# Kernel tuning notes

Hardware: AMD Instinct MI355X
Metric: run time of the kernel (lower is better)

Reference implementation:

```python
import jax, jax.numpy as jnp
import numpy as np

I_DIM = 50000
D_DIM = 128
N_EDGES = 800000
N_NODES = I_DIM + 1


def setup_inputs() -> dict:
    key = jax.random.key(0)
    k1, k2, k3, k4 = jax.random.split(key, 4)
    # edge[:,0] must be sorted for the original bincount+repeat normalization to be valid
    src = jnp.sort(jax.random.randint(k1, (N_EDGES,), 0, N_NODES))
    dst = jax.random.randint(k2, (N_EDGES,), 0, N_NODES)
    edge = jnp.stack([src, dst], axis=1).astype(jnp.int64)
    # GlorotNormal-style init for the embedding table and dense layers
    emb_mat = jax.random.normal(k3, (N_NODES, D_DIM), dtype=jnp.float32) * np.sqrt(2.0 / (N_NODES + D_DIM))
    kA, kB = jax.random.split(k4)
    W_scale = jax.random.normal(kA, (D_DIM, D_DIM), dtype=jnp.float32) * np.sqrt(2.0 / (2 * D_DIM))
    b_scale = jnp.zeros((D_DIM,), dtype=jnp.float32)
    W_att = jax.random.normal(kB, (2 * D_DIM, 1), dtype=jnp.float32) * np.sqrt(2.0 / (2 * D_DIM + 1))
    b_att = jnp.zeros((1,), dtype=jnp.float32)
    return {"edge": edge, "emb_mat": emb_mat, "W_scale": W_scale,
            "b_scale": b_scale, "W_att": W_att, "b_att": b_att}


def reference(edge, emb_mat, W_scale, b_scale, W_att, b_att):
    E = edge.shape[0]
    src = edge[:, 0]
    dst = edge[:, 1]
    # gather both endpoints, project: [E, 2, d]
    edge_emb = jnp.einsum('epd,df->epf', emb_mat[edge], W_scale) + b_scale
    edge_emb = edge_emb.reshape(E, -1)                       # [E, 2d]
    att = edge_emb @ W_att + b_att                           # [E, 1]
    att = jnp.where(att >= 0, att, 0.2 * att)                # LeakyReLU(0.2)
    att = jnp.squeeze(att, axis=-1)                          # [E]
    scores = jnp.exp(att - 1.0)
    score_sum = jax.ops.segment_sum(scores, src, num_segments=N_NODES)
    score_norm = scores / score_sum[src]                     # segment softmax
    item_scaled = emb_mat @ W_scale + b_scale                # [N, d]
    msgs = score_norm[:, None] * item_scaled[dst]            # [E, d]
    agg = jax.ops.segment_sum(msgs, src, num_segments=N_NODES)
    return jax.nn.sigmoid(agg)                               # [N, d]
```

## Files before the change

### kernel.cpp

```cpp
#include <hip/hip_runtime.h>
#include <math.h>

#define NN 50001
#define DD 128
#define NE 800000

typedef __attribute__((ext_vector_type(8))) short short8;
typedef __attribute__((ext_vector_type(4))) float floatx4;

__device__ __forceinline__ unsigned short f2bf(float f) {
    unsigned u = __builtin_bit_cast(unsigned, f);
    u += 0x7fffu + ((u >> 16) & 1u);
    return (unsigned short)(u >> 16);
}
__device__ __forceinline__ float bflo(unsigned u) {
    return __builtin_bit_cast(float, u << 16);
}
__device__ __forceinline__ float bfhi(unsigned u) {
    return __builtin_bit_cast(float, u & 0xffff0000u);
}
__device__ __forceinline__ float score(float att) {
    att = att >= 0.f ? att : 0.2f * att;
    return __expf(att - 1.f);
}

__global__ void k_prep(const float* __restrict__ W, unsigned short* __restrict__ WT,
                       const int* __restrict__ edge, int* __restrict__ row_ptr) {
    int b = blockIdx.x;
    if (b < 64) {
        int idx = b * 256 + threadIdx.x;
        int k = idx >> 7, j = idx & 127;
        WT[j * DD + k] = f2bf(W[idx]);
    } else {
        int e = (b - 64) * 256 + threadIdx.x;
        if (e >= NE) return;
        int s = edge[2 * e];
        if (e == 0) {
            for (int n = 0; n <= s; n++) row_ptr[n] = 0;
        } else {
            int p = edge[2 * (e - 1)];
            for (int n = p + 1; n <= s; n++) row_ptr[n] = e;
        }
        if (e == NE - 1) {
            for (int n = s + 1; n <= NN; n++) row_ptr[n] = NE;
        }
    }
}

__global__ void __launch_bounds__(256) k_gemm(const float* __restrict__ emb,
        const unsigned short* __restrict__ WT, const float* __restrict__ b_scale,
        const float* __restrict__ W_att, unsigned short* __restrict__ item,
        float* __restrict__ a_src, float* __restrict__ a_dst) {
    int wave = blockIdx.x * 4 + (threadIdx.x >> 6);
    int lane = threadIdx.x & 63;
    int base = wave * 16;
    if (base >= NN) return;
    int m = lane & 15, q = lane >> 4;

    int row = base + m; if (row >= NN) row = NN - 1;
    const float* ap = emb + (long)row * DD + q * 8;
    short8 a[4];
    #pragma unroll
    for (int ks = 0; ks < 4; ks++) {
        float4 f0 = *(const float4*)(ap + ks * 32);
        float4 f1 = *(const float4*)(ap + ks * 32 + 4);
        a[ks][0] = (short)f2bf(f0.x); a[ks][1] = (short)f2bf(f0.y);
        a[ks][2] = (short)f2bf(f0.z); a[ks][3] = (short)f2bf(f0.w);
        a[ks][4] = (short)f2bf(f1.x); a[ks][5] = (short)f2bf(f1.y);
        a[ks][6] = (short)f2bf(f1.z); a[ks][7] = (short)f2bf(f1.w);
    }

    float p_src[4] = {0.f, 0.f, 0.f, 0.f};
    float p_dst[4] = {0.f, 0.f, 0.f, 0.f};

    #pragma unroll
    for (int ft = 0; ft < 8; ft++) {
        int col = ft * 16 + m;
        floatx4 acc = {0.f, 0.f, 0.f, 0.f};
        #pragma unroll
        for (int ks = 0; ks < 4; ks++) {
            short8 b = *(const short8*)(WT + col * DD + ks * 32 + q * 8);
            acc = __builtin_amdgcn_mfma_f32_16x16x32_bf16(a[ks], b, acc, 0, 0, 0);
        }
        float bs = b_scale[col];
        float wsrc = W_att[col], wdst = W_att[DD + col];
        #pragma unroll
        for (int r = 0; r < 4; r++) {
            float v = acc[r] + bs;
            int gr = base + q * 4 + r;
            if (gr < NN) item[(long)gr * DD + col] = f2bf(v);
            p_src[r] += v * wsrc;
            p_dst[r] += v * wdst;
        }
    }
    #pragma unroll
    for (int off = 1; off <= 8; off <<= 1) {
        #pragma unroll
        for (int r = 0; r < 4; r++) {
            p_src[r] += __shfl_xor(p_src[r], off, 64);
            p_dst[r] += __shfl_xor(p_dst[r], off, 64);
        }
    }
    if (m == 0) {
        #pragma unroll
        for (int r = 0; r < 4; r++) {
            int gr = base + q * 4 + r;
            if (gr < NN) { a_src[gr] = p_src[r]; a_dst[gr] = p_dst[r]; }
        }
    }
}

__global__ void __launch_bounds__(256) k_agg(const int* __restrict__ edge,
        const int* __restrict__ row_ptr, const unsigned short* __restrict__ item,
        const float* __restrict__ a_src, const float* __restrict__ a_dst,
        const float* __restrict__ b_att, float* __restrict__ out) {
    int n = blockIdx.x * 4 + (threadIdx.x >> 6);
    int lane = threadIdx.x & 63;
    if (n >= NN) return;
    int g = lane >> 4, t = lane & 15;

    int start = row_ptr[n];
    int len = row_ptr[n + 1] - start;
    const int* dp = edge + 2 * start + 1;

    if (len > 0) {
        float asrc = a_src[n] + b_att[0];
        float acc[8] = {0.f, 0.f, 0.f, 0.f, 0.f, 0.f, 0.f, 0.f};
        float ssum = 0.f;
        int j = g;
        for (; j + 12 < len; j += 16) {
            int d0 = dp[2 * j], d1 = dp[2 * (j + 4)], d2 = dp[2 * (j + 8)], d3 = dp[2 * (j + 12)];
            float x0 = a_dst[d0], x1 = a_dst[d1], x2 = a_dst[d2], x3 = a_dst[d3];
            uint4 u0 = *(const uint4*)(item + (long)d0 * DD + t * 8);
            uint4 u1 = *(const uint4*)(item + (long)d1 * DD + t * 8);
            uint4 u2 = *(const uint4*)(item + (long)d2 * DD + t * 8);
            uint4 u3 = *(const uint4*)(item + (long)d3 * DD + t * 8);
            float s0 = score(asrc + x0), s1 = score(asrc + x1);
            float s2 = score(asrc + x2), s3 = score(asrc + x3);
            ssum += (s0 + s1) + (s2 + s3);
            acc[0] += s0 * bflo(u0.x); acc[1] += s0 * bfhi(u0.x);
            acc[2] += s0 * bflo(u0.y); acc[3] += s0 * bfhi(u0.y);
            acc[4] += s0 * bflo(u0.z); acc[5] += s0 * bfhi(u0.z);
            acc[6] += s0 * bflo(u0.w); acc[7] += s0 * bfhi(u0.w);
            acc[0] += s1 * bflo(u1.x); acc[1] += s1 * bfhi(u1.x);
            acc[2] += s1 * bflo(u1.y); acc[3] += s1 * bfhi(u1.y);
            acc[4] += s1 * bflo(u1.z); acc[5] += s1 * bfhi(u1.z);
            acc[6] += s1 * bflo(u1.w); acc[7] += s1 * bfhi(u1.w);
            acc[0] += s2 * bflo(u2.x); acc[1] += s2 * bfhi(u2.x);
            acc[2] += s2 * bflo(u2.y); acc[3] += s2 * bfhi(u2.y);
            acc[4] += s2 * bflo(u2.z); acc[5] += s2 * bfhi(u2.z);
            acc[6] += s2 * bflo(u2.w); acc[7] += s2 * bfhi(u2.w);
            acc[0] += s3 * bflo(u3.x); acc[1] += s3 * bfhi(u3.x);
            acc[2] += s3 * bflo(u3.y); acc[3] += s3 * bfhi(u3.y);
            acc[4] += s3 * bflo(u3.z); acc[5] += s3 * bfhi(u3.z);
            acc[6] += s3 * bflo(u3.w); acc[7] += s3 * bfhi(u3.w);
        }
        for (; j < len; j += 4) {
            int d = dp[2 * j];
            float x = a_dst[d];
            uint4 u = *(const uint4*)(item + (long)d * DD + t * 8);
            float s = score(asrc + x);
            ssum += s;
            acc[0] += s * bflo(u.x); acc[1] += s * bfhi(u.x);
            acc[2] += s * bflo(u.y); acc[3] += s * bfhi(u.y);
            acc[4] += s * bflo(u.z); acc[5] += s * bfhi(u.z);
            acc[6] += s * bflo(u.w); acc[7] += s * bfhi(u.w);
        }
        #pragma unroll
        for (int off = 16; off <= 32; off <<= 1) {
            #pragma unroll
            for (int k = 0; k < 8; k++) acc[k] += __shfl_xor(acc[k], off, 64);
            ssum += __shfl_xor(ssum, off, 64);
        }
        float inv = 1.f / ssum;
        float4 o;
        if (g == 0) {
            o.x = 1.f / (1.f + __expf(-acc[0] * inv));
            o.y = 1.f / (1.f + __expf(-acc[1] * inv));
            o.z = 1.f / (1.f + __expf(-acc[2] * inv));
            o.w = 1.f / (1.f + __expf(-acc[3] * inv));
            *(float4*)(out + (long)n * DD + t * 8) = o;
        } else if (g == 1) {
            o.x = 1.f / (1.f + __expf(-acc[4] * inv));
            o.y = 1.f / (1.f + __expf(-acc[5] * inv));
            o.z = 1.f / (1.f + __expf(-acc[6] * inv));
            o.w = 1.f / (1.f + __expf(-acc[7] * inv));
            *(float4*)(out + (long)n * DD + t * 8 + 4) = o;
        }
    } else {
        float4 h = make_float4(0.5f, 0.5f, 0.5f, 0.5f);
        if (g == 0)      *(float4*)(out + (long)n * DD + t * 8) = h;
        else if (g == 1) *(float4*)(out + (long)n * DD + t * 8 + 4) = h;
    }
}

extern "C" void kernel_launch(void* const* d_in, const int* in_sizes, int n_in,
                              void* d_out, int out_size, void* d_ws, size_t ws_size,
                              hipStream_t stream) {
    const int*   edge    = (const int*)d_in[0];
    const float* emb     = (const float*)d_in[1];
    const float* W_scale = (const float*)d_in[2];
    const float* b_scale = (const float*)d_in[3];
    const float* W_att   = (const float*)d_in[4];
    const float* b_att   = (const float*)d_in[5];
    float* out = (float*)d_out;

    char* ws = (char*)d_ws;
    unsigned short* WT      = (unsigned short*)(ws);
    int*            row_ptr = (int*)(ws + 32768);
    float*          a_src   = (float*)(ws + 233600);
    float*          a_dst   = (float*)(ws + 433792);
    unsigned short* item    = (unsigned short*)(ws + 633984);

    int node_blocks = (NN + 3) / 4;
    int tile_blocks = ((NN + 15) / 16 + 3) / 4;
    int edge_blocks = (NE + 255) / 256;

    k_prep <<<64 + edge_blocks, 256, 0, stream>>>(W_scale, WT, edge, row_ptr);
    k_gemm <<<tile_blocks,      256, 0, stream>>>(emb, WT, b_scale, W_att, item, a_src, a_dst);
    k_agg  <<<node_blocks,      256, 0, stream>>>(edge, row_ptr, item, a_src, a_dst, b_att, out);
}
```

Baseline: 146.8 us.

## Move row_ptr build into GEMM launch and transpose MFMA operands for vector stores

Row-pointer construction now runs in extra blocks of the GEMM kernel instead of the prep kernel, so the prep kernel only transposes W and the heavy edge scan overlaps with the GEMM. The MFMA operands are swapped so each lane holds four consecutive output features of one node. That allows packed 8-byte bf16 stores of item, float4 loads of bias and attention weights, and a shorter cross-lane reduction. The GEMM launch grows, and GEMM and edge blocks now compete for the same CUs.

```diff
diff --git a/kernel.cpp b/kernel.cpp
--- a/kernel.cpp
+++ b/kernel.cpp
@@ -4,6 +4,8 @@
 #define NN 50001
 #define DD 128
 #define NE 800000
+#define GEMM_BLOCKS 782
+#define EDGE_BLOCKS 3125
 
 typedef __attribute__((ext_vector_type(8))) short short8;
 typedef __attribute__((ext_vector_type(4))) float floatx4;
@@ -24,15 +26,19 @@
     return __expf(att - 1.f);
 }
 
-__global__ void k_prep(const float* __restrict__ W, unsigned short* __restrict__ WT,
-                       const int* __restrict__ edge, int* __restrict__ row_ptr) {
-    int b = blockIdx.x;
-    if (b < 64) {
-        int idx = b * 256 + threadIdx.x;
-        int k = idx >> 7, j = idx & 127;
-        WT[j * DD + k] = f2bf(W[idx]);
-    } else {
-        int e = (b - 64) * 256 + threadIdx.x;
+__global__ void k_prep(const float* __restrict__ W, unsigned short* __restrict__ WT) {
+    int idx = blockIdx.x * 256 + threadIdx.x;
+    int k = idx >> 7, j = idx & 127;
+    WT[j * DD + k] = f2bf(W[idx]);
+}
+
+__global__ void __launch_bounds__(256) k_gemm(const float* __restrict__ emb,
+        const unsigned short* __restrict__ WT, const float* __restrict__ b_scale,
+        const float* __restrict__ W_att, const int* __restrict__ edge,
+        unsigned short* __restrict__ item, float* __restrict__ a_src,
+        float* __restrict__ a_dst, int* __restrict__ row_ptr) {
+    if (blockIdx.x >= GEMM_BLOCKS) {
+        int e = (blockIdx.x - GEMM_BLOCKS) * 256 + threadIdx.x;
         if (e >= NE) return;
         int s = edge[2 * e];
         if (e == 0) {
@@ -44,70 +50,58 @@
         if (e == NE - 1) {
             for (int n = s + 1; n <= NN; n++) row_ptr[n] = NE;
         }
-    }
-}
-
-__global__ void __launch_bounds__(256) k_gemm(const float* __restrict__ emb,
-        const unsigned short* __restrict__ WT, const float* __restrict__ b_scale,
-        const float* __restrict__ W_att, unsigned short* __restrict__ item,
-        float* __restrict__ a_src, float* __restrict__ a_dst) {
+        return;
+    }
     int wave = blockIdx.x * 4 + (threadIdx.x >> 6);
     int lane = threadIdx.x & 63;
     int base = wave * 16;
     if (base >= NN) return;
     int m = lane & 15, q = lane >> 4;
-
-    int row = base + m; if (row >= NN) row = NN - 1;
-    const float* ap = emb + (long)row * DD + q * 8;
-    short8 a[4];
+    int node = base + m;
+    bool valid = node < NN;
+
+    int row = valid ? node : NN - 1;
+    const float* bp = emb + (long)row * DD + q * 8;
+    short8 b[4];
     #pragma unroll
     for (int ks = 0; ks < 4; ks++) {
-        float4 f0 = *(const float4*)(ap + ks * 32);
-        float4 f1 = *(const float4*)(ap + ks * 32 + 4);
-        a[ks][0] = (short)f2bf(f0.x); a[ks][1] = (short)f2bf(f0.y);
-        a[ks][2] = (short)f2bf(f0.z); a[ks][3] = (short)f2bf(f0.w);
-        a[ks][4] = (short)f2bf(f1.x); a[ks][5] = (short)f2bf(f1.y);
-        a[ks][6] = (short)f2bf(f1.z); a[ks][7] = (short)f2bf(f1.w);
-    }
-
-    float p_src[4] = {0.f, 0.f, 0.f, 0.f};
-    float p_dst[4] = {0.f, 0.f, 0.f, 0.f};
+        float4 f0 = *(const float4*)(bp + ks * 32);
+        float4 f1 = *(const float4*)(bp + ks * 32 + 4);
+        b[ks][0] = (short)f2bf(f0.x); b[ks][1] = (short)f2bf(f0.y);
+        b[ks][2] = (short)f2bf(f0.z); b[ks][3] = (short)f2bf(f0.w);
+        b[ks][4] = (short)f2bf(f1.x); b[ks][5] = (short)f2bf(f1.y);
+        b[ks][6] = (short)f2bf(f1.z); b[ks][7] = (short)f2bf(f1.w);
+    }
+
+    float p_src = 0.f, p_dst = 0.f;
 
     #pragma unroll
     for (int ft = 0; ft < 8; ft++) {
-        int col = ft * 16 + m;
         floatx4 acc = {0.f, 0.f, 0.f, 0.f};
+        const unsigned short* wrow = WT + (ft * 16 + m) * DD;
         #pragma unroll
         for (int ks = 0; ks < 4; ks++) {
-            short8 b = *(const short8*)(WT + col * DD + ks * 32 + q * 8);
-            acc = __builtin_amdgcn_mfma_f32_16x16x32_bf16(a[ks], b, acc, 0, 0, 0);
-        }
-        float bs = b_scale[col];
-        float wsrc = W_att[col], wdst = W_att[DD + col];
-        #pragma unroll
-        for (int r = 0; r < 4; r++) {
-            float v = acc[r] + bs;
-            int gr = base + q * 4 + r;
-            if (gr < NN) item[(long)gr * DD + col] = f2bf(v);
-            p_src[r] += v * wsrc;
-            p_dst[r] += v * wdst;
-        }
-    }
-    #pragma unroll
-    for (int off = 1; off <= 8; off <<= 1) {
-        #pragma unroll
-        for (int r = 0; r < 4; r++) {
-            p_src[r] += __shfl_xor(p_src[r], off, 64);
-            p_dst[r] += __shfl_xor(p_dst[r], off, 64);
-        }
-    }
-    if (m == 0) {
-        #pragma unroll
-        for (int r = 0; r < 4; r++) {
-            int gr = base + q * 4 + r;
-            if (gr < NN) { a_src[gr] = p_src[r]; a_dst[gr] = p_dst[r]; }
-        }
-    }
+            short8 a = *(const short8*)(wrow + ks * 32 + q * 8);
+            acc = __builtin_amdgcn_mfma_f32_16x16x32_bf16(a, b[ks], acc, 0, 0, 0);
+        }
+        int fo = ft * 16 + q * 4;
+        float4 bs = *(const float4*)(b_scale + fo);
+        float4 ws = *(const float4*)(W_att + fo);
+        float4 wd = *(const float4*)(W_att + DD + fo);
+        float v0 = acc[0] + bs.x, v1 = acc[1] + bs.y;
+        float v2 = acc[2] + bs.z, v3 = acc[3] + bs.w;
+        if (valid) {
+            uint2 pk;
+            pk.x = (unsigned)f2bf(v0) | ((unsigned)f2bf(v1) << 16);
+            pk.y = (unsigned)f2bf(v2) | ((unsigned)f2bf(v3) << 16);
+            *(uint2*)(item + (long)node * DD + fo) = pk;
+        }
+        p_src += v0 * ws.x + v1 * ws.y + v2 * ws.z + v3 * ws.w;
+        p_dst += v0 * wd.x + v1 * wd.y + v2 * wd.z + v3 * wd.w;
+    }
+    p_src += __shfl_xor(p_src, 16, 64); p_src += __shfl_xor(p_src, 32, 64);
+    p_dst += __shfl_xor(p_dst, 16, 64); p_dst += __shfl_xor(p_dst, 32, 64);
+    if (q == 0 && valid) { a_src[node] = p_src; a_dst[node] = p_dst; }
 }
 
 __global__ void __launch_bounds__(256) k_agg(const int* __restrict__ edge,
@@ -213,10 +207,10 @@
     unsigned short* item    = (unsigned short*)(ws + 633984);
 
     int node_blocks = (NN + 3) / 4;
-    int tile_blocks = ((NN + 15) / 16 + 3) / 4;
-    int edge_blocks = (NE + 255) / 256;
-
-    k_prep <<<64 + edge_blocks, 256, 0, stream>>>(W_scale, WT, edge, row_ptr);
-    k_gemm <<<tile_blocks,      256, 0, stream>>>(emb, WT, b_scale, W_att, item, a_src, a_dst);
-    k_agg  <<<node_blocks,      256, 0, stream>>>(edge, row_ptr, item, a_src, a_dst, b_att, out);
-}
+
+    k_prep <<<64,                        256, 0, stream>>>(W_scale, WT);
+    k_gemm <<<GEMM_BLOCKS + EDGE_BLOCKS, 256, 0, stream>>>(emb, WT, b_scale, W_att,
+                                                           edge, item, a_src, a_dst, row_ptr);
+    k_agg  <<<node_blocks,               256, 0, stream>>>(edge, row_ptr, item,
+                                                           a_src, a_dst, b_att, out);
+}
```

After: 145.1 us. About the same (-1.1%).
